# Kernel tuning notes

Measured on AMD Instinct MI355X. Metric: run time of the kernel, lower is better.

## Reference

```python
import jax, jax.numpy as jnp
import numpy as np

B, S, HID = 2, 2048, 2048
H, KV, D = 32, 4, 128
G = H // KV
EPS = 1e-6
SCALE = D ** -0.5
ROPE_THETA = 1000000.0


def setup_inputs() -> dict:
    key = jax.random.key(0)
    ks = jax.random.split(key, 6)
    hidden_states = jax.random.normal(ks[0], (B, S, HID), jnp.float32)
    # real RoPE tables (position_embeddings passed into forward)
    inv_freq = 1.0 / (ROPE_THETA ** (np.arange(0, D, 2, dtype=np.float32) / D))
    ang = np.arange(S, dtype=np.float32)[:, None] * inv_freq[None, :]  # [S, D/2]
    emb = np.concatenate([ang, ang], axis=-1)  # [S, D]
    cos = jnp.broadcast_to(jnp.asarray(np.cos(emb)), (B, S, D))
    sin = jnp.broadcast_to(jnp.asarray(np.sin(emb)), (B, S, D))
    sd = 0.02
    wq = jax.random.normal(ks[1], (H * D, HID), jnp.float32) * sd
    wk = jax.random.normal(ks[2], (KV * D, HID), jnp.float32) * sd
    wv = jax.random.normal(ks[3], (KV * D, HID), jnp.float32) * sd
    wo = jax.random.normal(ks[4], (HID, H * D), jnp.float32) * sd
    q_norm_w = jnp.ones((D,), jnp.float32)
    k_norm_w = jnp.ones((D,), jnp.float32)
    return {"hidden_states": hidden_states, "cos": cos, "sin": sin,
            "wq": wq, "wk": wk, "wv": wv, "wo": wo,
            "q_norm_w": q_norm_w, "k_norm_w": k_norm_w}


def _rms_norm(x, w):
    var = jnp.mean(jnp.square(x), axis=-1, keepdims=True)
    return x * jax.lax.rsqrt(var + EPS) * w


def _rotate_half(x):
    x1, x2 = jnp.split(x, 2, axis=-1)
    return jnp.concatenate([-x2, x1], axis=-1)


def _rope(x, cos, sin):
    # x: [B,S,N,D]; cos/sin: [B,S,1,D] (unsqueeze_dim=2)
    return x * cos + _rotate_half(x) * sin


def reference(hidden_states, cos, sin, wq, wk, wv, wo, q_norm_w, k_norm_w):
    x = hidden_states
    q = jnp.einsum('bsh,oh->bso', x, wq).reshape(B, S, H, D)
    k = jnp.einsum('bsh,oh->bso', x, wk).reshape(B, S, KV, D)
    v = jnp.einsum('bsh,oh->bso', x, wv).reshape(B, S, KV, D)
    q = _rms_norm(q, q_norm_w)
    k = _rms_norm(k, k_norm_w)
    c = cos[:, :, None, :]
    s = sin[:, :, None, :]
    q = _rope(q, c, s)
    k = _rope(k, c, s)
    # GQA causal attention, BSND layout
    qg = q.reshape(B, S, KV, G, D)
    scores = jnp.einsum('bqkgd,bskd->bkgqs', qg, k) * SCALE  # [B,KV,G,Sq,Sk]
    causal = jnp.tril(jnp.ones((S, S), bool))
    scores = jnp.where(causal, scores, jnp.finfo(scores.dtype).min)
    p = jax.nn.softmax(scores, axis=-1)
    out = jnp.einsum('bkgqs,bskd->bqkgd', p, v).reshape(B, S, H * D)
    return jnp.einsum('bso,ho->bsh', out, wo)
```

## Files before the change

### kernel.cpp

```cpp
#include <hip/hip_runtime.h>
#include <hip/hip_bf16.h>

typedef __attribute__((ext_vector_type(8))) short short8;
typedef __attribute__((ext_vector_type(4))) float f32x4;

#define DEVI static __device__ __forceinline__

constexpr int Bb = 2, Ss = 2048, Hh = 32, KVc = 4, Dc = 128;
constexpr float EPSc = 1e-6f;
constexpr float SCALEc = 0.08838834764831845f;
constexpr float LOG2Ec = 1.4426950408889634f;
constexpr float SCALE2c = SCALEc * LOG2Ec;

DEVI float bf2f(short s) {
  unsigned u = ((unsigned)(unsigned short)s) << 16;
  float f; __builtin_memcpy(&f, &u, 4); return f;
}
DEVI short f2bf(float f) {
  __hip_bfloat16 h = __float2bfloat16(f);
  unsigned short u; __builtin_memcpy(&u, &h, 2); return (short)u;
}
DEVI float ex2(float x) {
  float r; asm("v_exp_f32 %0, %1" : "=v"(r) : "v"(x)); return r;
}

#define GLDS(gsrc, ldst) __builtin_amdgcn_global_load_lds( \
    (const __attribute__((address_space(1))) void*)(gsrc), \
    (__attribute__((address_space(3))) void*)(ldst), 16, 0, 0)

struct Cvt5 { const float* src[5]; short* dst[5]; };
__global__ void cvt_all(Cvt5 a) {
  constexpr int CUM[6] = {0, 2097152, 4194304, 4456448, 4718592, 6815744};
  const int stride = gridDim.x * blockDim.x;
  for (int i = blockIdx.x * blockDim.x + threadIdx.x; i < 6815744; i += stride) {
    int s = 0;
#pragma unroll
    for (int t = 1; t < 5; ++t) if (i >= CUM[t]) s = t;
    int j = i - CUM[s];
    float4 v = ((const float4*)a.src[s])[j];
    short4 o;
    o.x = f2bf(v.x); o.y = f2bf(v.y); o.z = f2bf(v.z); o.w = f2bf(v.w);
    ((short4*)a.dst[s])[j] = o;
  }
}

__launch_bounds__(512, 2)
__global__ void gemm8q(const short* __restrict__ A,
                       const short* __restrict__ Bp,
                       short* __restrict__ oq,
                       const float* __restrict__ cosb,
                       const float* __restrict__ sinb,
                       const float* __restrict__ qnw,
                       int K)
{
  __shared__ short lA[2][256 * 64];
  __shared__ short lB[2][256 * 64];

  const int tid = threadIdx.x, lane = tid & 63;
  const int wvi = tid >> 6;
  const int l15 = lane & 15, g = lane >> 4;
  const int wm = wvi >> 1, wn = wvi & 1;
  const int m0 = blockIdx.x * 256;
  const int n0 = blockIdx.y * 256;

  f32x4 acc[4][8] = {};

  auto stA = [&](int half, int slot, int kt) {
#pragma unroll
    for (int j = 0; j < 2; ++j) {
      int rr = j * 64 + (tid >> 3);
      int grow = ((rr >> 5) << 6) + half * 32 + (rr & 31);
      GLDS(A + (size_t)(m0 + grow) * K + kt * 64 + (((tid & 7) ^ (rr & 7)) << 3),
           &lA[slot][(half * 128 + j * 64) * 64 + tid * 8]);
    }
  };
  auto stB = [&](int half, int slot, int kt) {
#pragma unroll
    for (int j = 0; j < 2; ++j) {
      int rr = j * 64 + (tid >> 3);
      int gn = ((rr >> 6) << 7) + half * 64 + (rr & 63);
      GLDS(Bp + (size_t)(n0 + gn) * K + kt * 64 + (((tid & 7) ^ (rr & 7)) << 3),
           &lB[slot][(half * 128 + j * 64) * 64 + tid * 8]);
    }
  };

#define PH(SLOT, MH, NH, STG, GT) do {                                          \
    short8 afr[2][2], bfr[4][2];                                                \
    _Pragma("unroll")                                                           \
    for (int mi2 = 0; mi2 < 2; ++mi2) {                                         \
      int rp = (MH) * 128 + wm * 32 + mi2 * 16 + l15;                           \
      _Pragma("unroll")                                                         \
      for (int kk = 0; kk < 2; ++kk)                                            \
        afr[mi2][kk] = *(const short8*)(&lA[SLOT][rp * 64 +                     \
                         (((kk * 4 + g) ^ (rp & 7)) << 3)]);                    \
    }                                                                           \
    _Pragma("unroll")                                                           \
    for (int nj = 0; nj < 4; ++nj) {                                            \
      int rp = (NH) * 128 + wn * 64 + nj * 16 + l15;                            \
      _Pragma("unroll")                                                         \
      for (int kk = 0; kk < 2; ++kk)                                            \
        bfr[nj][kk] = *(const short8*)(&lB[SLOT][rp * 64 +                      \
                         (((kk * 4 + g) ^ (rp & 7)) << 3)]);                    \
    }                                                                           \
    STG;                                                                        \
    asm volatile("" ::: "memory");                                              \
    __builtin_amdgcn_s_barrier();                                               \
    __builtin_amdgcn_s_setprio(1);                                              \
    _Pragma("unroll")                                                           \
    for (int mi2 = 0; mi2 < 2; ++mi2)                                           \
      _Pragma("unroll")                                                         \
      for (int nj = 0; nj < 4; ++nj)                                            \
        _Pragma("unroll")                                                       \
        for (int kk = 0; kk < 2; ++kk)                                          \
          acc[(MH)*2 + mi2][(NH)*4 + nj] =                                      \
            __builtin_amdgcn_mfma_f32_16x16x32_bf16(afr[mi2][kk], bfr[nj][kk],  \
                acc[(MH)*2 + mi2][(NH)*4 + nj], 0, 0, 0);                       \
    __builtin_amdgcn_s_setprio(0);                                              \
    GT;                                                                         \
    asm volatile("" ::: "memory");                                              \
    __builtin_amdgcn_s_barrier();                                               \
  } while (0)

  const int nit = K >> 7;

  stA(0, 0, 0); stB(0, 0, 0); stA(1, 0, 0); stB(1, 0, 0);
  stA(0, 1, 1); stB(0, 1, 1);
  asm volatile("s_waitcnt vmcnt(4)" ::: "memory");
  __builtin_amdgcn_s_barrier();

  for (int it = 0; it < nit; ++it) {
    const int kt1 = 2 * it + 1;
    const int k2 = 2 * it + 2, k3 = 2 * it + 3;
    const bool pre = (it + 1 < nit);
    PH(0, 0, 0, { stA(1, 1, kt1); }, {});
    PH(0, 0, 1, { stB(1, 1, kt1); }, {});
    PH(0, 1, 0, { if (pre) stA(0, 0, k2); }, {});
    PH(0, 1, 1, { if (pre) stB(0, 0, k2); },
               { if (pre) asm volatile("s_waitcnt vmcnt(4)" ::: "memory");
                 else     asm volatile("s_waitcnt vmcnt(0)" ::: "memory"); });
    PH(1, 0, 0, { if (pre) stA(1, 0, k2); }, {});
    PH(1, 0, 1, { if (pre) stB(1, 0, k2); }, {});
    PH(1, 1, 0, { if (pre) stA(0, 1, k3); }, {});
    PH(1, 1, 1, { if (pre) stB(0, 1, k3); },
               { if (pre) asm volatile("s_waitcnt vmcnt(4)" ::: "memory"); });
  }
#undef PH

  float w8[8];
#pragma unroll
  for (int ni = 0; ni < 8; ++ni) w8[ni] = qnw[ni * 16 + l15];
#pragma unroll
  for (int mi = 0; mi < 4; ++mi)
#pragma unroll
    for (int r = 0; r < 4; ++r) {
      int m = m0 + wm * 64 + mi * 16 + g * 4 + r;
      int b = m >> 11, s = m & 2047;
      float xv[8];
      float ssq = 0.f;
#pragma unroll
      for (int ni = 0; ni < 8; ++ni) { xv[ni] = acc[mi][ni][r]; ssq += xv[ni] * xv[ni]; }
      ssq += __shfl_xor(ssq, 1);
      ssq += __shfl_xor(ssq, 2);
      ssq += __shfl_xor(ssq, 4);
      ssq += __shfl_xor(ssq, 8);
      float inv = rsqrtf(ssq * (1.0f / 128.0f) + EPSc);
      float xn[8];
#pragma unroll
      for (int ni = 0; ni < 8; ++ni) xn[ni] = xv[ni] * inv * w8[ni];
      const float* cpr = cosb + ((size_t)b * Ss + s) * Dc;
      const float* spr = sinb + ((size_t)b * Ss + s) * Dc;
#pragma unroll
      for (int ni = 0; ni < 8; ++ni) {
        int d = ni * 16 + l15;
        float c = cpr[d], sn = spr[d];
        float rot = (ni < 4) ? -xn[ni + 4] : xn[ni - 4];
        float o = xn[ni] * c + rot * sn;
        oq[(size_t)m * 4096 + n0 + wn * 128 + d] = f2bf(o * SCALE2c);
      }
    }
}

template<int MODE>
__launch_bounds__(256, 4)
__global__ void gemm2(const short* __restrict__ A,
                      const short* __restrict__ B1,
                      const short* __restrict__ B2,
                      short* __restrict__ ok,
                      short* __restrict__ ov,
                      float* __restrict__ of,
                      const float* __restrict__ cosb,
                      const float* __restrict__ sinb,
                      const float* __restrict__ knw,
                      int K)
{
  __shared__ short lA[2][128 * 32];
  __shared__ short lB[2][128 * 32];
  const int tid = threadIdx.x;
  const int lane = tid & 63;
  const int wvi = tid >> 6;
  const int l15 = lane & 15, g = lane >> 4;
  const int m0 = blockIdx.x * 128;
  const int nt = blockIdx.y;
  const short* Bp; int n0, region;
  if (MODE == 0) {
    if (nt < 4) { Bp = B1; n0 = nt * 128;       region = 1; }
    else        { Bp = B2; n0 = (nt - 4) * 128; region = 2; }
  } else { Bp = B1; n0 = nt * 128; region = 3; }

  const int wrow = wvi * 32;
  const int srow = tid >> 2, schunk = tid & 3;

  f32x4 acc[2][8] = {};

  auto STAGE = [&](int ks, int bufi) {
    const int k0 = ks * 32;
#pragma unroll
    for (int c = 0; c < 2; ++c) {
      int row = c * 64 + srow;
      int gc = schunk ^ ((row >> 1) & 3);
      GLDS(A  + (size_t)(m0 + row) * K + k0 + gc * 8, &lA[bufi][(c * 256 + tid) * 8]);
      GLDS(Bp + (size_t)(n0 + row) * K + k0 + gc * 8, &lB[bufi][(c * 256 + tid) * 8]);
    }
  };

  const int nks = K >> 5;
  STAGE(0, 0);
  STAGE(1, 1);

  for (int ks = 0; ks < nks; ++ks) {
    const int cb = ks & 1;
    if (ks + 1 < nks) asm volatile("s_waitcnt vmcnt(4)" ::: "memory");
    else              asm volatile("s_waitcnt vmcnt(0)" ::: "memory");
    __builtin_amdgcn_s_barrier();
    asm volatile("" ::: "memory");

    short8 afr[2], bfr[8];
#pragma unroll
    for (int i = 0; i < 2; ++i) {
      int ra = wrow + i * 16 + l15;
      afr[i] = *(const short8*)(&lA[cb][0] + ra * 32 + ((g ^ ((ra >> 1) & 3)) * 8));
    }
#pragma unroll
    for (int i = 0; i < 8; ++i) {
      int rb = i * 16 + l15;
      bfr[i] = *(const short8*)(&lB[cb][0] + rb * 32 + ((g ^ ((rb >> 1) & 3)) * 8));
    }
#pragma unroll
    for (int mi = 0; mi < 2; ++mi)
#pragma unroll
      for (int ni = 0; ni < 8; ++ni)
        acc[mi][ni] = __builtin_amdgcn_mfma_f32_16x16x32_bf16(afr[mi], bfr[ni], acc[mi][ni], 0, 0, 0);

    asm volatile("" ::: "memory");
    __builtin_amdgcn_s_barrier();
    if (ks + 2 < nks) STAGE(ks + 2, cb);
  }

  if (MODE == 1) {
#pragma unroll
    for (int mi = 0; mi < 2; ++mi)
#pragma unroll
      for (int r = 0; r < 4; ++r) {
        int m = m0 + wrow + mi * 16 + g * 4 + r;
#pragma unroll
        for (int ni = 0; ni < 8; ++ni)
          of[(size_t)m * 2048 + n0 + ni * 16 + l15] = acc[mi][ni][r];
      }
  } else if (region == 2) {
#pragma unroll
    for (int mi = 0; mi < 2; ++mi)
#pragma unroll
      for (int r = 0; r < 4; ++r) {
        int m = m0 + wrow + mi * 16 + g * 4 + r;
        int b = m >> 11, s = m & 2047;
#pragma unroll
        for (int ni = 0; ni < 8; ++ni) {
          int n = n0 + ni * 16 + l15;
          int kvi = n >> 7, d = n & 127;
          ov[(((size_t)b * KVc + kvi) * 128 + d) * Ss + s] = f2bf(acc[mi][ni][r]);
        }
      }
  } else {
    float w8[8];
#pragma unroll
    for (int ni = 0; ni < 8; ++ni) w8[ni] = knw[ni * 16 + l15];
#pragma unroll
    for (int mi = 0; mi < 2; ++mi)
#pragma unroll
      for (int r = 0; r < 4; ++r) {
        int m = m0 + wrow + mi * 16 + g * 4 + r;
        int b = m >> 11, s = m & 2047;
        float xv[8];
        float ssq = 0.f;
#pragma unroll
        for (int ni = 0; ni < 8; ++ni) { xv[ni] = acc[mi][ni][r]; ssq += xv[ni] * xv[ni]; }
        ssq += __shfl_xor(ssq, 1);
        ssq += __shfl_xor(ssq, 2);
        ssq += __shfl_xor(ssq, 4);
        ssq += __shfl_xor(ssq, 8);
        float inv = rsqrtf(ssq * (1.0f / 128.0f) + EPSc);
        float xn[8];
#pragma unroll
        for (int ni = 0; ni < 8; ++ni) xn[ni] = xv[ni] * inv * w8[ni];
        const float* cpr = cosb + ((size_t)b * Ss + s) * Dc;
        const float* spr = sinb + ((size_t)b * Ss + s) * Dc;
#pragma unroll
        for (int ni = 0; ni < 8; ++ni) {
          int dl = ni * 16 + l15;
          float c = cpr[dl], sn = spr[dl];
          float rot = (ni < 4) ? -xn[ni + 4] : xn[ni - 4];
          float o = xn[ni] * c + rot * sn;
          int n = n0 + dl;
          int kvi = n >> 7, d = n & 127;
          ok[(((size_t)b * KVc + kvi) * Ss + s) * 128 + d] = f2bf(o);
        }
      }
  }
}

__launch_bounds__(256, 2)
__global__ void attn_fwd(const short* __restrict__ qb,
                         const short* __restrict__ kbuf,
                         const short* __restrict__ vtbuf,
                         short* __restrict__ ob)
{
  __shared__ short lK[2][64 * 128];
  __shared__ short lV[2][128 * 64];
  __shared__ short lP[4][32 * 32];
  const int tid = threadIdx.x, lane = tid & 63, wvi = tid >> 6;
  const int l15 = lane & 15, g = lane >> 4;
  const int pi = blockIdx.x, h = blockIdx.y, b = blockIdx.z;
  const int kv = h >> 3;
  const short* kp = kbuf  + ((size_t)b * KVc + kv) * Ss * 128;
  const short* vp = vtbuf + ((size_t)b * KVc + kv) * 128 * Ss;
  const int krow = tid >> 4, kch = tid & 15;
  const int vrow = tid >> 3, vch = tid & 7;

  for (int which = 0; which < 2; ++which) {
    const int qt = which ? (15 - pi) : pi;
    const int qwb = qt * 128 + (wvi & 3) * 32;
    const int nkt = 2 * qt + 2;

    short8 qf[2][4];
#pragma unroll
    for (int qs = 0; qs < 2; ++qs)
#pragma unroll
      for (int dc = 0; dc < 4; ++dc)
        qf[qs][dc] = *(const short8*)(qb + (size_t)(b * Ss + qwb + qs * 16 + l15) * 4096
                                         + h * 128 + dc * 32 + g * 8);

    f32x4 oacc[2][8] = {};
    float mrun[2] = { -__builtin_inff(), -__builtin_inff() };
    float lrun[2] = { 0.f, 0.f };

    auto STAGE = [&](int kt, int bufi) {
      const int kb0 = kt * 64;
#pragma unroll
      for (int c = 0; c < 4; ++c) {
        int r = c * 16 + krow;
        int gc = kch ^ (r & 7);
        GLDS(kp + (size_t)(kb0 + r) * 128 + gc * 8, &lK[bufi][(c * 256 + tid) * 8]);
      }
#pragma unroll
      for (int c = 0; c < 4; ++c) {
        int r = c * 32 + vrow;
        int gc = vch ^ (r & 7);
        GLDS(vp + (size_t)r * Ss + kb0 + gc * 8, &lV[bufi][(c * 256 + tid) * 8]);
      }
    };

    STAGE(0, 0);
    STAGE(1, 1);

    for (int kt = 0; kt < nkt; ++kt) {
      const int cb = kt & 1;
      if (kt + 1 < nkt) asm volatile("s_waitcnt vmcnt(8)" ::: "memory");
      else              asm volatile("s_waitcnt vmcnt(0)" ::: "memory");
      __builtin_amdgcn_s_barrier();
      asm volatile("" ::: "memory");

#pragma unroll
      for (int half = 0; half < 2; ++half) {
        const int kb0 = kt * 64 + half * 32;
        if (kb0 <= qwb + 31) {
          short8 kf[2][4];
#pragma unroll
          for (int ks = 0; ks < 2; ++ks)
#pragma unroll
            for (int dc = 0; dc < 4; ++dc) {
              int row = half * 32 + ks * 16 + l15;
              kf[ks][dc] = *(const short8*)(&lK[cb][0] + row * 128 + (((dc * 4 + g) ^ (row & 7)) * 8));
            }
          f32x4 st[2][2] = {};
          __builtin_amdgcn_s_setprio(1);
#pragma unroll
          for (int qs = 0; qs < 2; ++qs)
#pragma unroll
            for (int ks = 0; ks < 2; ++ks)
#pragma unroll
              for (int dc = 0; dc < 4; ++dc)
                st[qs][ks] = __builtin_amdgcn_mfma_f32_16x16x32_bf16(kf[ks][dc], qf[qs][dc], st[qs][ks], 0, 0, 0);
          __builtin_amdgcn_s_setprio(0);

          const bool need_mask = (kb0 + 31 > qwb);
#pragma unroll
          for (int qs = 0; qs < 2; ++qs) {
            const int qg = qwb + qs * 16 + l15;
            float p[8];
            float tmax = -__builtin_inff();
#pragma unroll
            for (int ks = 0; ks < 2; ++ks)
#pragma unroll
              for (int r = 0; r < 4; ++r) {
                float v = st[qs][ks][r];
                if (need_mask && (kb0 + ks * 16 + g * 4 + r > qg)) v = -__builtin_inff();
                p[ks * 4 + r] = v;
                tmax = fmaxf(tmax, v);
              }
            tmax = fmaxf(tmax, __shfl_xor(tmax, 16));
            tmax = fmaxf(tmax, __shfl_xor(tmax, 32));
            float m_use = mrun[qs];
            if (__any(tmax > m_use + 11.0f)) {
              float mnew = fmaxf(m_use, tmax);
              float scl = ex2(m_use - mnew);
              lrun[qs] *= scl;
              mrun[qs] = mnew;
#pragma unroll
              for (int r = 0; r < 4; ++r) {
                float sc = __shfl(scl, g * 4 + r);
#pragma unroll
                for (int dt = 0; dt < 8; ++dt)
                  oacc[qs][dt][r] *= sc;
              }
              m_use = mnew;
            }
            float rsum = 0.f;
#pragma unroll
            for (int j = 0; j < 8; ++j) { p[j] = ex2(p[j] - m_use); rsum += p[j]; }
            rsum += __shfl_xor(rsum, 16);
            rsum += __shfl_xor(rsum, 32);
            lrun[qs] += rsum;
            {
              int row = qs * 16 + l15;
              int sw = (row >> 1) & 3;
              short* pr = lP[wvi] + row * 32;
#pragma unroll
              for (int ks = 0; ks < 2; ++ks) {
                int idx = (((2 * ks + (g >> 1)) ^ sw) * 8) + (g & 1) * 4;
                short4 pw;
                pw.x = f2bf(p[ks * 4 + 0]);
                pw.y = f2bf(p[ks * 4 + 1]);
                pw.z = f2bf(p[ks * 4 + 2]);
                pw.w = f2bf(p[ks * 4 + 3]);
                *(short4*)(pr + idx) = pw;
              }
            }
          }
          asm volatile("" ::: "memory");
          short8 vf[8];
#pragma unroll
          for (int dt = 0; dt < 8; ++dt) {
            int row = dt * 16 + l15;
            vf[dt] = *(const short8*)(&lV[cb][0] + row * 64 + (((half * 4 + g) ^ (row & 7)) * 8));
          }
          __builtin_amdgcn_s_setprio(1);
#pragma unroll
          for (int qs = 0; qs < 2; ++qs) {
            int row = qs * 16 + l15;
            short8 pf = *(const short8*)(lP[wvi] + row * 32 + ((g ^ ((row >> 1) & 3)) * 8));
#pragma unroll
            for (int dt = 0; dt < 8; ++dt)
              oacc[qs][dt] = __builtin_amdgcn_mfma_f32_16x16x32_bf16(pf, vf[dt], oacc[qs][dt], 0, 0, 0);
          }
          __builtin_amdgcn_s_setprio(0);
          asm volatile("" ::: "memory");
        }
      }

      asm volatile("" ::: "memory");
      __builtin_amdgcn_s_barrier();
      if (kt + 2 < nkt) STAGE(kt + 2, cb);
    }

#pragma unroll
    for (int qs = 0; qs < 2; ++qs)
#pragma unroll
      for (int r = 0; r < 4; ++r) {
        float inv = 1.0f / __shfl(lrun[qs], g * 4 + r);
        int qrow = qwb + qs * 16 + g * 4 + r;
        short* op = ob + (size_t)(b * Ss + qrow) * 4096 + h * 128;
#pragma unroll
        for (int dt = 0; dt < 8; ++dt)
          op[dt * 16 + l15] = f2bf(oacc[qs][dt][r] * inv);
      }
  }
}

extern "C" void kernel_launch(void* const* d_in, const int* in_sizes, int n_in,
                              void* d_out, int out_size, void* d_ws, size_t ws_size,
                              hipStream_t stream) {
  const float* x    = (const float*)d_in[0];
  const float* cosb = (const float*)d_in[1];
  const float* sinb = (const float*)d_in[2];
  const float* wq   = (const float*)d_in[3];
  const float* wk   = (const float*)d_in[4];
  const float* wv   = (const float*)d_in[5];
  const float* wo   = (const float*)d_in[6];
  const float* qw   = (const float*)d_in[7];
  const float* kw   = (const float*)d_in[8];

  size_t off = 0;
  auto alloc = [&](size_t bytes) {
    char* p = (char*)d_ws + off;
    off += (bytes + 255) & ~(size_t)255;
    return p;
  };
  short* x_bf  = (short*)alloc((size_t)8388608 * 2);
  short* wq_bf = (short*)alloc((size_t)8388608 * 2);
  short* wk_bf = (short*)alloc((size_t)1048576 * 2);
  short* wv_bf = (short*)alloc((size_t)1048576 * 2);
  short* wo_bf = (short*)alloc((size_t)8388608 * 2);
  short* q_bf  = (short*)alloc((size_t)16777216 * 2);
  short* k_bf  = (short*)alloc((size_t)2097152 * 2);
  short* v_bf  = (short*)alloc((size_t)2097152 * 2);
  short* ao_bf = (short*)alloc((size_t)16777216 * 2);

  Cvt5 ca;
  ca.src[0] = x;    ca.dst[0] = x_bf;
  ca.src[1] = wq;   ca.dst[1] = wq_bf;
  ca.src[2] = wk;   ca.dst[2] = wk_bf;
  ca.src[3] = wv;   ca.dst[3] = wv_bf;
  ca.src[4] = wo;   ca.dst[4] = wo_bf;
  cvt_all<<<2048, 256, 0, stream>>>(ca);

  gemm8q<<<dim3(16, 16), 512, 0, stream>>>(x_bf, wq_bf, q_bf, cosb, sinb, qw, 2048);
  gemm2<0><<<dim3(32, 8), 256, 0, stream>>>(x_bf, wk_bf, wv_bf, k_bf, v_bf, nullptr,
                                            cosb, sinb, kw, 2048);
  attn_fwd<<<dim3(8, 32, 2), 256, 0, stream>>>(q_bf, k_bf, v_bf, ao_bf);
  gemm2<1><<<dim3(32, 16), 256, 0, stream>>>(ao_bf, wo_bf, nullptr, nullptr, nullptr,
                                             (float*)d_out, nullptr, nullptr, nullptr, 4096);
}
```

Baseline: 342.6 us.

## Replace output projection GEMM with 8-wave 128x256 pipelined kernel

Adds a dedicated gemm8o kernel for the output projection. It uses 512 threads, a 128x256 tile with K-step 64 and XOR-swizzled LDS, and prefetches half-tiles inside eight phases per iteration with setprio around the MFMAs. It replaces the generic 128x128, 256-thread gemm2<1> path and removes the MODE template from gemm2. The aim is more operand reuse per LDS load and better overlap of global loads with MFMA. The cost is higher register and LDS pressure, and a grid of only 256 blocks.

```diff
diff --git a/kernel.cpp b/kernel.cpp
--- a/kernel.cpp
+++ b/kernel.cpp
@@ -180,14 +180,119 @@
     }
 }
 
-template<int MODE>
+__launch_bounds__(512, 2)
+__global__ void gemm8o(const short* __restrict__ A,
+                       const short* __restrict__ Bp,
+                       float* __restrict__ of)
+{
+  constexpr int K = 4096;
+  __shared__ short lA[2][128 * 64];
+  __shared__ short lB[2][256 * 64];
+
+  const int tid = threadIdx.x, lane = tid & 63;
+  const int wvi = tid >> 6;
+  const int l15 = lane & 15, g = lane >> 4;
+  const int wm = wvi >> 2, wn = wvi & 3;
+  const int m0 = blockIdx.x * 128;
+  const int n0 = blockIdx.y * 256;
+
+  f32x4 acc[4][4] = {};
+
+  auto stA = [&](int half, int slot, int kt) {
+    int rr = tid >> 3;
+    int grow = ((rr >> 5) << 6) + half * 32 + (rr & 31);
+    GLDS(A + (size_t)(m0 + grow) * K + kt * 64 + (((tid & 7) ^ (rr & 7)) << 3),
+         &lA[slot][(half * 64) * 64 + tid * 8]);
+  };
+  auto stB = [&](int half, int slot, int kt) {
+#pragma unroll
+    for (int j = 0; j < 2; ++j) {
+      int rr = j * 64 + (tid >> 3);
+      int gn = ((rr >> 5) << 6) + half * 32 + (rr & 31);
+      GLDS(Bp + (size_t)(n0 + gn) * K + kt * 64 + (((tid & 7) ^ (rr & 7)) << 3),
+           &lB[slot][(half * 128 + j * 64) * 64 + tid * 8]);
+    }
+  };
+
+#define PH(SLOT, MH, NH, STG, GT) do {                                          \
+    short8 afr[2][2], bfr[2][2];                                                \
+    _Pragma("unroll")                                                           \
+    for (int mi2 = 0; mi2 < 2; ++mi2) {                                         \
+      int rp = (MH) * 64 + wm * 32 + mi2 * 16 + l15;                            \
+      _Pragma("unroll")                                                         \
+      for (int kk = 0; kk < 2; ++kk)                                            \
+        afr[mi2][kk] = *(const short8*)(&lA[SLOT][rp * 64 +                     \
+                         (((kk * 4 + g) ^ (rp & 7)) << 3)]);                    \
+    }                                                                           \
+    _Pragma("unroll")                                                           \
+    for (int nj = 0; nj < 2; ++nj) {                                            \
+      int rp = (NH) * 128 + wn * 32 + nj * 16 + l15;                            \
+      _Pragma("unroll")                                                         \
+      for (int kk = 0; kk < 2; ++kk)                                            \
+        bfr[nj][kk] = *(const short8*)(&lB[SLOT][rp * 64 +                      \
+                         (((kk * 4 + g) ^ (rp & 7)) << 3)]);                    \
+    }                                                                           \
+    STG;                                                                        \
+    asm volatile("" ::: "memory");                                              \
+    __builtin_amdgcn_s_barrier();                                               \
+    __builtin_amdgcn_s_setprio(1);                                              \
+    _Pragma("unroll")                                                           \
+    for (int mi2 = 0; mi2 < 2; ++mi2)                                           \
+      _Pragma("unroll")                                                         \
+      for (int nj = 0; nj < 2; ++nj)                                            \
+        _Pragma("unroll")                                                       \
+        for (int kk = 0; kk < 2; ++kk)                                          \
+          acc[(MH)*2 + mi2][(NH)*2 + nj] =                                      \
+            __builtin_amdgcn_mfma_f32_16x16x32_bf16(afr[mi2][kk], bfr[nj][kk],  \
+                acc[(MH)*2 + mi2][(NH)*2 + nj], 0, 0, 0);                       \
+    __builtin_amdgcn_s_setprio(0);                                              \
+    GT;                                                                         \
+    asm volatile("" ::: "memory");                                              \
+    __builtin_amdgcn_s_barrier();                                               \
+  } while (0)
+
+  const int nit = K >> 7;
+
+  stA(0, 0, 0); stB(0, 0, 0); stA(1, 0, 0); stB(1, 0, 0);
+  stA(0, 1, 1); stB(0, 1, 1);
+  asm volatile("s_waitcnt vmcnt(3)" ::: "memory");
+  __builtin_amdgcn_s_barrier();
+
+  for (int it = 0; it < nit; ++it) {
+    const int kt1 = 2 * it + 1;
+    const int k2 = 2 * it + 2, k3 = 2 * it + 3;
+    const bool pre = (it + 1 < nit);
+    PH(0, 0, 0, { stA(1, 1, kt1); }, {});
+    PH(0, 0, 1, { stB(1, 1, kt1); }, {});
+    PH(0, 1, 0, { if (pre) stA(0, 0, k2); }, {});
+    PH(0, 1, 1, { if (pre) stB(0, 0, k2); },
+               { if (pre) asm volatile("s_waitcnt vmcnt(3)" ::: "memory");
+                 else     asm volatile("s_waitcnt vmcnt(0)" ::: "memory"); });
+    PH(1, 0, 0, { if (pre) stA(1, 0, k2); }, {});
+    PH(1, 0, 1, { if (pre) stB(1, 0, k2); }, {});
+    PH(1, 1, 0, { if (pre) stA(0, 1, k3); }, {});
+    PH(1, 1, 1, { if (pre) stB(0, 1, k3); },
+               { if (pre) asm volatile("s_waitcnt vmcnt(3)" ::: "memory"); });
+  }
+#undef PH
+
+#pragma unroll
+  for (int mi = 0; mi < 4; ++mi)
+#pragma unroll
+    for (int r = 0; r < 4; ++r) {
+      int m = m0 + wm * 64 + mi * 16 + g * 4 + r;
+#pragma unroll
+      for (int ni = 0; ni < 4; ++ni)
+        of[(size_t)m * 2048 + n0 + wn * 64 + ni * 16 + l15] = acc[mi][ni][r];
+    }
+}
+
 __launch_bounds__(256, 4)
 __global__ void gemm2(const short* __restrict__ A,
                       const short* __restrict__ B1,
                       const short* __restrict__ B2,
                       short* __restrict__ ok,
                       short* __restrict__ ov,
-                      float* __restrict__ of,
                       const float* __restrict__ cosb,
                       const float* __restrict__ sinb,
                       const float* __restrict__ knw,
@@ -202,10 +307,8 @@
   const int m0 = blockIdx.x * 128;
   const int nt = blockIdx.y;
   const short* Bp; int n0, region;
-  if (MODE == 0) {
-    if (nt < 4) { Bp = B1; n0 = nt * 128;       region = 1; }
-    else        { Bp = B2; n0 = (nt - 4) * 128; region = 2; }
-  } else { Bp = B1; n0 = nt * 128; region = 3; }
+  if (nt < 4) { Bp = B1; n0 = nt * 128;       region = 1; }
+  else        { Bp = B2; n0 = (nt - 4) * 128; region = 2; }
 
   const int wrow = wvi * 32;
   const int srow = tid >> 2, schunk = tid & 3;
@@ -256,17 +359,7 @@
     if (ks + 2 < nks) STAGE(ks + 2, cb);
   }
 
-  if (MODE == 1) {
-#pragma unroll
-    for (int mi = 0; mi < 2; ++mi)
-#pragma unroll
-      for (int r = 0; r < 4; ++r) {
-        int m = m0 + wrow + mi * 16 + g * 4 + r;
-#pragma unroll
-        for (int ni = 0; ni < 8; ++ni)
-          of[(size_t)m * 2048 + n0 + ni * 16 + l15] = acc[mi][ni][r];
-      }
-  } else if (region == 2) {
+  if (region == 2) {
 #pragma unroll
     for (int mi = 0; mi < 2; ++mi)
 #pragma unroll
@@ -534,9 +627,8 @@
   cvt_all<<<2048, 256, 0, stream>>>(ca);
 
   gemm8q<<<dim3(16, 16), 512, 0, stream>>>(x_bf, wq_bf, q_bf, cosb, sinb, qw, 2048);
-  gemm2<0><<<dim3(32, 8), 256, 0, stream>>>(x_bf, wk_bf, wv_bf, k_bf, v_bf, nullptr,
-                                            cosb, sinb, kw, 2048);
+  gemm2<<<dim3(32, 8), 256, 0, stream>>>(x_bf, wk_bf, wv_bf, k_bf, v_bf,
+                                         cosb, sinb, kw, 2048);
   attn_fwd<<<dim3(8, 32, 2), 256, 0, stream>>>(q_bf, k_bf, v_bf, ao_bf);
-  gemm2<1><<<dim3(32, 16), 256, 0, stream>>>(ao_bf, wo_bf, nullptr, nullptr, nullptr,
-                                             (float*)d_out, nullptr, nullptr, nullptr, 4096);
-}
+  gemm8o<<<dim3(32, 8), 512, 0, stream>>>(ao_bf, wo_bf, (float*)d_out);
+}
```

New measurement: 347.4 us. Within noise of the previous version (+1.4%).
